# Kernel optimization log

Measured on AMD Instinct MI355X. Metric: run time of the kernel, lower is better.

The kernel has to match this reference:

```python
import jax, jax.numpy as jnp
import numpy as np

DIM = 1024
NUM_HEADS = 16
HEAD_DIM = DIM // NUM_HEADS
SCALE = HEAD_DIM ** -0.5


def setup_inputs() -> dict:
    key = jax.random.key(0)
    k1, k2, k3 = jax.random.split(key, 3)
    B, N = 2, 2048
    x = jax.random.normal(k1, (B, N, DIM), dtype=jnp.float32)
    # qkv: Linear(dim, 3*dim, bias=False); proj: Linear(dim, dim) with bias
    w_qkv = jax.random.normal(k2, (3 * DIM, DIM), dtype=jnp.float32) * (DIM ** -0.5)
    w_proj = jax.random.normal(k3, (DIM, DIM), dtype=jnp.float32) * (DIM ** -0.5)
    b_proj = jnp.zeros((DIM,), dtype=jnp.float32)
    return {"x": x, "w_qkv": w_qkv, "w_proj": w_proj, "b_proj": b_proj}


def reference(x, w_qkv, w_proj, b_proj):
    B, N, C = x.shape
    H, D = NUM_HEADS, HEAD_DIM
    qkv = jnp.einsum('bnc,fc->bnf', x, w_qkv)                 # [B,N,3C]
    qkv = qkv.reshape(B, N, 3, H, D).transpose(2, 0, 3, 1, 4)  # [3,B,H,N,D]
    q, k, v = qkv[0], qkv[1], qkv[2]
    q = q * SCALE
    attn = jnp.einsum('bhnd,bhmd->bhnm', q, k)                 # [B,H,N,N]
    attn = jax.nn.softmax(attn, axis=-1)
    out = jnp.einsum('bhnm,bhmd->bhnd', attn, v)               # [B,H,N,D]
    out = out.transpose(0, 2, 1, 3).reshape(B, N, C)
    out = jnp.einsum('bnc,fc->bnf', out, w_proj) + b_proj
    return out
```

## Files before the change

kernel.cpp:

```cpp
#include <hip/hip_runtime.h>
#include <hip/hip_bf16.h>
#include <stdint.h>

typedef __attribute__((ext_vector_type(4))) float f32x4;
typedef __attribute__((ext_vector_type(16))) float f32x16;
typedef __attribute__((ext_vector_type(8))) short bf16x8;
typedef __attribute__((ext_vector_type(4))) short bf16x4;
typedef unsigned short ushort_t;

#define QSCALE 0.18033688f

__device__ inline short f2bf(float f) {
  unsigned u = __builtin_bit_cast(unsigned, f);
  u += 0x7fffu + ((u >> 16) & 1u);
  return (short)(u >> 16);
}

__device__ inline void gload_lds16(const void* g, void* l) {
  __builtin_amdgcn_global_load_lds(
      (const __attribute__((address_space(1))) void*)g,
      (__attribute__((address_space(3))) void*)l, 16, 0, 0);
}

__device__ inline unsigned cvtpk(float a, float b) {
  unsigned r;
  asm("v_cvt_pk_bf16_f32 %0, %1, %2" : "=v"(r) : "v"(a), "v"(b));
  return r;
}

__device__ inline void swap32u(unsigned& a, unsigned& b) {
  asm("v_permlane32_swap_b32 %0, %1" : "+v"(a), "+v"(b));
}

__global__ __launch_bounds__(256) void cvt_all(const float* __restrict__ x,
                                               const float* __restrict__ wq,
                                               const float* __restrict__ wp,
                                               short* __restrict__ Xb,
                                               short* __restrict__ Wq,
                                               short* __restrict__ Wp) {
  int i = blockIdx.x * 256 + threadIdx.x;
  const float* s;
  short* d;
  int off;
  if (i < 524288)       { s = x;  d = Xb; off = i; }
  else if (i < 917504)  { s = wq; d = Wq; off = i - 524288; }
  else                  { s = wp; d = Wp; off = i - 917504; }
  const float4* sv = (const float4*)s;
  float4 a = sv[2 * off], b = sv[2 * off + 1];
  bf16x8 o;
  o[0] = f2bf(a.x); o[1] = f2bf(a.y); o[2] = f2bf(a.z); o[3] = f2bf(a.w);
  o[4] = f2bf(b.x); o[5] = f2bf(b.y); o[6] = f2bf(b.z); o[7] = f2bf(b.w);
  ((bf16x8*)d)[off] = o;
}

template <int BN, int F32OUT, int SPLITV>
__global__ __launch_bounds__(256, 3) void gemm_pipe(const short* __restrict__ A,
                                                    const short* __restrict__ B,
                                                    void* __restrict__ Cv,
                                                    short* __restrict__ Vtg,
                                                    const float* __restrict__ bias,
                                                    int scale_cols, float scale_val,
                                                    int M, int N, int K) {
  constexpr int MFR = (BN == 128) ? 4 : 2;
  __shared__ short Abuf[3][128 * 32];
  __shared__ short Bbuf[3][BN * 32];
  const int tid = threadIdx.x, wv = tid >> 6, ln = tid & 63;
  const int wm = (BN == 128) ? (wv >> 1) : wv;
  const int wn = (BN == 128) ? (wv & 1) : 0;
  const int bn0 = blockIdx.x * BN, bm0 = blockIdx.y * 128;
  const int nt = K >> 5;

  const int srow = ln >> 2;
  const int scol = (((ln & 3) ^ (srow & 3)) * 8);
  const int fln = ln & 15;
  const int fk = ln >> 4;

  f32x4 acc[MFR][4] = {};

  auto stage = [&](int t, int s) {
    const size_t k0 = (size_t)(t << 5);
#pragma unroll
    for (int rd = 0; rd < 2; rd++) {
      int ch = 2 * wv + rd;
      gload_lds16(A + (size_t)(bm0 + ch * 16 + srow) * K + k0 + scol,
                  (char*)Abuf[s] + ch * 1024);
    }
    if constexpr (BN == 128) {
#pragma unroll
      for (int rd = 0; rd < 2; rd++) {
        int ch = 2 * wv + rd;
        gload_lds16(B + (size_t)(bn0 + ch * 16 + srow) * K + k0 + scol,
                    (char*)Bbuf[s] + ch * 1024);
      }
    } else {
      gload_lds16(B + (size_t)(bn0 + wv * 16 + srow) * K + k0 + scol,
                  (char*)Bbuf[s] + wv * 1024);
    }
  };

  stage(0, 0);
  stage(1, 1);
  if constexpr (BN == 128) asm volatile("s_waitcnt vmcnt(4)" ::: "memory");
  else                     asm volatile("s_waitcnt vmcnt(3)" ::: "memory");
  __builtin_amdgcn_s_barrier();
  __builtin_amdgcn_sched_barrier(0);

  for (int t = 0; t < nt; t++) {
    const int s = t % 3;
    const bool more = (t + 2) < nt;
    if (more) stage(t + 2, (t + 2) % 3);

    const char* Ab = (const char*)Abuf[s];
    const char* Bb = (const char*)Bbuf[s];
    bf16x8 af[MFR], bfr[4];
#pragma unroll
    for (int m = 0; m < MFR; m++) {
      int R = wm * (MFR * 16) + m * 16 + fln;
      af[m] = *(const bf16x8*)(Ab + R * 64 + ((fk ^ (R & 3)) << 4));
    }
#pragma unroll
    for (int n = 0; n < 4; n++) {
      int R = wn * 64 + n * 16 + fln;
      bfr[n] = *(const bf16x8*)(Bb + R * 64 + ((fk ^ (R & 3)) << 4));
    }

    __builtin_amdgcn_s_setprio(1);
#pragma unroll
    for (int m = 0; m < MFR; m++)
#pragma unroll
      for (int n = 0; n < 4; n++)
        acc[m][n] = __builtin_amdgcn_mfma_f32_16x16x32_bf16(af[m], bfr[n], acc[m][n], 0, 0, 0);
    __builtin_amdgcn_s_setprio(0);

    if (more) {
      if constexpr (BN == 128) asm volatile("s_waitcnt vmcnt(4)" ::: "memory");
      else                     asm volatile("s_waitcnt vmcnt(3)" ::: "memory");
    } else {
      asm volatile("s_waitcnt vmcnt(0)" ::: "memory");
    }
    __builtin_amdgcn_s_barrier();
    __builtin_amdgcn_sched_barrier(0);
  }

  const int r0 = bm0 + wm * (MFR * 16), c0 = bn0 + wn * 64;
  const int fg4 = (ln >> 4) * 4;
#pragma unroll
  for (int m = 0; m < MFR; m++) {
    const int row0 = r0 + m * 16 + fg4;
#pragma unroll
    for (int n = 0; n < 4; n++) {
      const int col = c0 + n * 16 + fln;
      if constexpr (SPLITV) {
        if (col < 2048) {
          const float sc = (col < scale_cols) ? scale_val : 1.0f;
#pragma unroll
          for (int j = 0; j < 4; j++)
            ((short*)Cv)[(size_t)(row0 + j) * 2048 + col] = f2bf(acc[m][n][j] * sc);
        } else {
          const int f = col - 2048, h = f >> 6, d = f & 63;
          const int bb = row0 >> 11, ntok = row0 & 2047;
          bf16x4 w;
#pragma unroll
          for (int j = 0; j < 4; j++) w[j] = f2bf(acc[m][n][j]);
          *(bf16x4*)(Vtg + ((size_t)((bb * 16 + h) * 64 + d)) * 2048 + ntok) = w;
        }
      } else {
#pragma unroll
        for (int j = 0; j < 4; j++) {
          float v = acc[m][n][j];
          if (col < scale_cols) v *= scale_val;
          if (F32OUT) ((float*)Cv)[(size_t)(row0 + j) * N + col] = v + bias[col];
          else        ((short*)Cv)[(size_t)(row0 + j) * N + col] = f2bf(v);
        }
      }
    }
  }
}

__global__ __launch_bounds__(256, 2) void attn_fwd(const short* __restrict__ QK,
                                                   const short* __restrict__ Vtg,
                                                   short* __restrict__ AO) {
  __shared__ short Ks[3][64 * 64];
  __shared__ short Vt[3][64 * 64];
  const int tid = threadIdx.x, wv = tid >> 6, ln = tid & 63;
  const int lq = ln & 31, hi = ln >> 5;
  const int id = blockIdx.x;
  const int c = (id & 7) * 64 + (id >> 3);
  const int qt = c & 15, bh = c >> 4;
  const int b = bh >> 4, h = bh & 15;
  const short* base = QK + (size_t)(b * 2048) * 2048 + h * 64;
  const short* Kg = base + 1024;
  const short* Vg = Vtg + (size_t)bh * 64 * 2048;
  const int qrow = qt * 128 + wv * 32 + lq;

  bf16x8 qf[4];
  {
    const short* Qrow = base + (size_t)qrow * 2048;
#pragma unroll
    for (int ds = 0; ds < 4; ds++)
      qf[ds] = *(const bf16x8*)(Qrow + ds * 16 + hi * 8);
  }

  const int krow = ln >> 3;
  const int kcol = ((ln & 7) ^ (ln >> 3)) * 8;

  float l_run = 0.f;
  f32x16 o0 = {}, o1 = {};

#define STAGE(t, s)                                                              \
  {                                                                              \
    _Pragma("unroll")                                                            \
    for (int rd = 0; rd < 2; rd++) {                                             \
      const int r8 = 16 * wv + 8 * rd + krow;                                    \
      gload_lds16(Kg + (size_t)((t) * 64 + r8) * 2048 + kcol,                    \
                  (char*)Ks[s] + (2 * wv + rd) * 1024);                          \
      gload_lds16(Vg + (size_t)r8 * 2048 + (t) * 64 + kcol,                      \
                  (char*)Vt[s] + (2 * wv + rd) * 1024);                          \
    }                                                                            \
  }

  STAGE(0, 0);
  STAGE(1, 1);

  for (int t = 0; t < 32; t++) {
    const int s = t % 3;
    if (t < 31) asm volatile("s_waitcnt vmcnt(4)" ::: "memory");
    else        asm volatile("s_waitcnt vmcnt(0)" ::: "memory");
    __builtin_amdgcn_s_barrier();
    __builtin_amdgcn_sched_barrier(0);
    if (t + 2 < 32) STAGE(t + 2, (t + 2) % 3);

    f32x16 c0 = {}, c1 = {};
    const char* Kb = (const char*)Ks[s];
    __builtin_amdgcn_s_setprio(1);
#pragma unroll
    for (int ds = 0; ds < 4; ds++) {
      const int cp = (ds * 2 + hi) ^ (lq & 7);
      bf16x8 ka0 = *(const bf16x8*)(Kb + lq * 128 + cp * 16);
      bf16x8 ka1 = *(const bf16x8*)(Kb + (32 + lq) * 128 + cp * 16);
      c0 = __builtin_amdgcn_mfma_f32_32x32x16_bf16(ka0, qf[ds], c0, 0, 0, 0);
      c1 = __builtin_amdgcn_mfma_f32_32x32x16_bf16(ka1, qf[ds], c1, 0, 0, 0);
    }
    __builtin_amdgcn_s_setprio(0);

#pragma unroll
    for (int r = 0; r < 16; r++) c0[r] = __builtin_amdgcn_exp2f(c0[r]);
#pragma unroll
    for (int r = 0; r < 16; r++) c1[r] = __builtin_amdgcn_exp2f(c1[r]);
    {
      float st[8];
#pragma unroll
      for (int r = 0; r < 8; r++)
        st[r] = (c0[2 * r] + c0[2 * r + 1]) + (c1[2 * r] + c1[2 * r + 1]);
#pragma unroll
      for (int r = 0; r < 4; r++) st[r] += st[r + 4];
      l_run += (st[0] + st[1]) + (st[2] + st[3]);
    }

    bf16x8 pa[4];
#pragma unroll
    for (int cs = 0; cs < 2; cs++) {
      const f32x16& p = cs ? c1 : c0;
#pragma unroll
      for (int ksl = 0; ksl < 2; ksl++) {
        unsigned A0 = cvtpk(p[8 * ksl + 0], p[8 * ksl + 1]);
        unsigned A1 = cvtpk(p[8 * ksl + 2], p[8 * ksl + 3]);
        unsigned B0 = cvtpk(p[8 * ksl + 4], p[8 * ksl + 5]);
        unsigned B1 = cvtpk(p[8 * ksl + 6], p[8 * ksl + 7]);
        swap32u(A0, B0);
        swap32u(A1, B1);
        union { unsigned u[4]; bf16x8 v; } tmp;
        tmp.u[0] = A0; tmp.u[1] = A1; tmp.u[2] = B0; tmp.u[3] = B1;
        pa[cs * 2 + ksl] = tmp.v;
      }
    }

    const char* Vb = (const char*)Vt[s];
    __builtin_amdgcn_s_setprio(1);
#pragma unroll
    for (int ks = 0; ks < 4; ks++) {
      const int cp = (ks * 2 + hi) ^ (lq & 7);
      bf16x8 va0 = *(const bf16x8*)(Vb + lq * 128 + cp * 16);
      bf16x8 va1 = *(const bf16x8*)(Vb + (32 + lq) * 128 + cp * 16);
      o0 = __builtin_amdgcn_mfma_f32_32x32x16_bf16(va0, pa[ks], o0, 0, 0, 0);
      o1 = __builtin_amdgcn_mfma_f32_32x32x16_bf16(va1, pa[ks], o1, 0, 0, 0);
    }
    __builtin_amdgcn_s_setprio(0);
  }
#undef STAGE

  l_run += __shfl_xor(l_run, 32);
  const float inv = __builtin_amdgcn_rcpf(l_run);
  short* Arow = AO + ((size_t)(b * 2048) + qrow) * 1024 + h * 64;
#pragma unroll
  for (int dt = 0; dt < 2; dt++) {
    const f32x16& o = dt ? o1 : o0;
#pragma unroll
    for (int g = 0; g < 4; g++) {
      bf16x4 w;
#pragma unroll
      for (int i = 0; i < 4; i++) w[i] = f2bf(o[4 * g + i] * inv);
      *(bf16x4*)(Arow + dt * 32 + 8 * g + 4 * hi) = w;
    }
  }
}

extern "C" void kernel_launch(void* const* d_in, const int* in_sizes, int n_in,
                              void* d_out, int out_size, void* d_ws, size_t ws_size,
                              hipStream_t stream) {
  const float* x = (const float*)d_in[0];
  const float* w_qkv = (const float*)d_in[1];
  const float* w_proj = (const float*)d_in[2];
  const float* b_proj = (const float*)d_in[3];
  float* out = (float*)d_out;

  char* ws = (char*)d_ws;
  short* Xb  = (short*)(ws + 0);
  short* Wq  = (short*)(ws + 8388608);
  short* Wp  = (short*)(ws + 14680064);
  short* QK  = (short*)(ws + 16777216);
  short* Vtg = (short*)(ws + 33554432);
  short* AO  = (short*)(ws + 41943040);

  cvt_all<<<4096, 256, 0, stream>>>(x, w_qkv, w_proj, Xb, Wq, Wp);

  gemm_pipe<128, 0, 1><<<dim3(24, 32), 256, 0, stream>>>(Xb, Wq, QK, Vtg, nullptr,
                                                         1024, QSCALE, 4096, 3072, 1024);

  attn_fwd<<<dim3(512), 256, 0, stream>>>(QK, Vtg, AO);

  gemm_pipe<64, 1, 0><<<dim3(16, 32), 256, 0, stream>>>(AO, Wp, out, nullptr, b_proj,
                                                        0, 1.0f, 4096, 1024, 1024);
}
```

Baseline: 114.4 us.

## Replace triple-buffered K=32 GEMM with double-buffered K=64 128x128 tiles

Both projection GEMMs now use one kernel that stages 64-wide K slices into two LDS buffers, with a wider 8-way XOR swizzle. Each stage issues twice as many MFMAs per barrier. The output projection moves from 128x64 to 128x128 tiles, halving its grid to 256 blocks. This cuts barrier and loop overhead and improves reuse per tile. In exchange it lowers occupancy (launch bounds 2), makes the prefetch shallower with an extra barrier per iteration, and leaves fewer blocks for the small projection GEMM on a GPU with many CUs.

```diff
diff --git a/kernel.cpp b/kernel.cpp
--- a/kernel.cpp
+++ b/kernel.cpp
@@ -53,99 +53,94 @@
   ((bf16x8*)d)[off] = o;
 }
 
-template <int BN, int F32OUT, int SPLITV>
-__global__ __launch_bounds__(256, 3) void gemm_pipe(const short* __restrict__ A,
-                                                    const short* __restrict__ B,
-                                                    void* __restrict__ Cv,
-                                                    short* __restrict__ Vtg,
-                                                    const float* __restrict__ bias,
-                                                    int scale_cols, float scale_val,
-                                                    int M, int N, int K) {
-  constexpr int MFR = (BN == 128) ? 4 : 2;
-  __shared__ short Abuf[3][128 * 32];
-  __shared__ short Bbuf[3][BN * 32];
+template <int F32OUT, int SPLITV>
+__global__ __launch_bounds__(256, 2) void gemm_db(const short* __restrict__ A,
+                                                  const short* __restrict__ B,
+                                                  void* __restrict__ Cv,
+                                                  short* __restrict__ Vtg,
+                                                  const float* __restrict__ bias,
+                                                  int scale_cols, float scale_val,
+                                                  int M, int N, int K) {
+  __shared__ short Ab[2][128 * 64];
+  __shared__ short Bb[2][128 * 64];
   const int tid = threadIdx.x, wv = tid >> 6, ln = tid & 63;
-  const int wm = (BN == 128) ? (wv >> 1) : wv;
-  const int wn = (BN == 128) ? (wv & 1) : 0;
-  const int bn0 = blockIdx.x * BN, bm0 = blockIdx.y * 128;
-  const int nt = K >> 5;
-
-  const int srow = ln >> 2;
-  const int scol = (((ln & 3) ^ (srow & 3)) * 8);
+  const int wm = wv >> 1, wn = wv & 1;
+  const int bn0 = blockIdx.x * 128, bm0 = blockIdx.y * 128;
+  const int nt = K >> 6;
+
+  const int srow = ln >> 3;
+  const int scol = ((ln & 7) ^ (ln >> 3)) * 8;
   const int fln = ln & 15;
   const int fk = ln >> 4;
 
-  f32x4 acc[MFR][4] = {};
+  f32x4 acc[4][4] = {};
 
   auto stage = [&](int t, int s) {
-    const size_t k0 = (size_t)(t << 5);
-#pragma unroll
-    for (int rd = 0; rd < 2; rd++) {
-      int ch = 2 * wv + rd;
-      gload_lds16(A + (size_t)(bm0 + ch * 16 + srow) * K + k0 + scol,
-                  (char*)Abuf[s] + ch * 1024);
-    }
-    if constexpr (BN == 128) {
-#pragma unroll
-      for (int rd = 0; rd < 2; rd++) {
-        int ch = 2 * wv + rd;
-        gload_lds16(B + (size_t)(bn0 + ch * 16 + srow) * K + k0 + scol,
-                    (char*)Bbuf[s] + ch * 1024);
-      }
-    } else {
-      gload_lds16(B + (size_t)(bn0 + wv * 16 + srow) * K + k0 + scol,
-                  (char*)Bbuf[s] + wv * 1024);
+    const size_t k0 = (size_t)t << 6;
+#pragma unroll
+    for (int rd = 0; rd < 4; rd++) {
+      const int ch = 4 * wv + rd;
+      gload_lds16(A + (size_t)(bm0 + ch * 8 + srow) * K + k0 + scol,
+                  (char*)Ab[s] + ch * 1024);
+      gload_lds16(B + (size_t)(bn0 + ch * 8 + srow) * K + k0 + scol,
+                  (char*)Bb[s] + ch * 1024);
     }
   };
 
   stage(0, 0);
   stage(1, 1);
-  if constexpr (BN == 128) asm volatile("s_waitcnt vmcnt(4)" ::: "memory");
-  else                     asm volatile("s_waitcnt vmcnt(3)" ::: "memory");
+  asm volatile("s_waitcnt vmcnt(8)" ::: "memory");
   __builtin_amdgcn_s_barrier();
   __builtin_amdgcn_sched_barrier(0);
 
   for (int t = 0; t < nt; t++) {
-    const int s = t % 3;
-    const bool more = (t + 2) < nt;
-    if (more) stage(t + 2, (t + 2) % 3);
-
-    const char* Ab = (const char*)Abuf[s];
-    const char* Bb = (const char*)Bbuf[s];
-    bf16x8 af[MFR], bfr[4];
-#pragma unroll
-    for (int m = 0; m < MFR; m++) {
-      int R = wm * (MFR * 16) + m * 16 + fln;
-      af[m] = *(const bf16x8*)(Ab + R * 64 + ((fk ^ (R & 3)) << 4));
+    const int s = t & 1;
+    const char* Ap = (const char*)Ab[s];
+    const char* Bp = (const char*)Bb[s];
+
+    bf16x8 af[4][2], bf[4][2];
+#pragma unroll
+    for (int m = 0; m < 4; m++) {
+      const int R = wm * 64 + m * 16 + fln;
+#pragma unroll
+      for (int kk = 0; kk < 2; kk++)
+        af[m][kk] = *(const bf16x8*)(Ap + R * 128 + ((((kk << 2) | fk) ^ (R & 7)) << 4));
     }
 #pragma unroll
     for (int n = 0; n < 4; n++) {
-      int R = wn * 64 + n * 16 + fln;
-      bfr[n] = *(const bf16x8*)(Bb + R * 64 + ((fk ^ (R & 3)) << 4));
+      const int R = wn * 64 + n * 16 + fln;
+#pragma unroll
+      for (int kk = 0; kk < 2; kk++)
+        bf[n][kk] = *(const bf16x8*)(Bp + R * 128 + ((((kk << 2) | fk) ^ (R & 7)) << 4));
     }
 
     __builtin_amdgcn_s_setprio(1);
 #pragma unroll
-    for (int m = 0; m < MFR; m++)
-#pragma unroll
-      for (int n = 0; n < 4; n++)
-        acc[m][n] = __builtin_amdgcn_mfma_f32_16x16x32_bf16(af[m], bfr[n], acc[m][n], 0, 0, 0);
+    for (int kk = 0; kk < 2; kk++)
+#pragma unroll
+      for (int m = 0; m < 4; m++)
+#pragma unroll
+        for (int n = 0; n < 4; n++)
+          acc[m][n] = __builtin_amdgcn_mfma_f32_16x16x32_bf16(af[m][kk], bf[n][kk], acc[m][n], 0, 0, 0);
     __builtin_amdgcn_s_setprio(0);
 
-    if (more) {
-      if constexpr (BN == 128) asm volatile("s_waitcnt vmcnt(4)" ::: "memory");
-      else                     asm volatile("s_waitcnt vmcnt(3)" ::: "memory");
-    } else {
-      asm volatile("s_waitcnt vmcnt(0)" ::: "memory");
-    }
-    __builtin_amdgcn_s_barrier();
-    __builtin_amdgcn_sched_barrier(0);
-  }
-
-  const int r0 = bm0 + wm * (MFR * 16), c0 = bn0 + wn * 64;
-  const int fg4 = (ln >> 4) * 4;
-#pragma unroll
-  for (int m = 0; m < MFR; m++) {
+    if (t + 1 < nt) {
+      __builtin_amdgcn_s_barrier();
+      if (t + 2 < nt) {
+        stage(t + 2, s);
+        asm volatile("s_waitcnt vmcnt(8)" ::: "memory");
+      } else {
+        asm volatile("s_waitcnt vmcnt(0)" ::: "memory");
+      }
+      __builtin_amdgcn_s_barrier();
+      __builtin_amdgcn_sched_barrier(0);
+    }
+  }
+
+  const int r0 = bm0 + wm * 64, c0 = bn0 + wn * 64;
+  const int fg4 = fk * 4;
+#pragma unroll
+  for (int m = 0; m < 4; m++) {
     const int row0 = r0 + m * 16 + fg4;
 #pragma unroll
     for (int n = 0; n < 4; n++) {
@@ -324,11 +319,11 @@
 
   cvt_all<<<4096, 256, 0, stream>>>(x, w_qkv, w_proj, Xb, Wq, Wp);
 
-  gemm_pipe<128, 0, 1><<<dim3(24, 32), 256, 0, stream>>>(Xb, Wq, QK, Vtg, nullptr,
-                                                         1024, QSCALE, 4096, 3072, 1024);
+  gemm_db<0, 1><<<dim3(24, 32), 256, 0, stream>>>(Xb, Wq, QK, Vtg, nullptr,
+                                                  1024, QSCALE, 4096, 3072, 1024);
 
   attn_fwd<<<dim3(512), 256, 0, stream>>>(QK, Vtg, AO);
 
-  gemm_pipe<64, 1, 0><<<dim3(16, 32), 256, 0, stream>>>(AO, Wp, out, nullptr, b_proj,
-                                                        0, 1.0f, 4096, 1024, 1024);
-}
+  gemm_db<1, 0><<<dim3(8, 32), 256, 0, stream>>>(AO, Wp, out, nullptr, b_proj,
+                                                 0, 1.0f, 4096, 1024, 1024);
+}
```

Measured after the change: 115.6 us. No clear change (+1.0%).
